# Optimization experiments

Hardware: AMD Instinct MI355X
Metric: run time of the kernel (lower is better)

The kernel has to match this reference:

```python
import jax, jax.numpy as jnp
import numpy as np
from jax.scipy.special import gammaln

NPTS = 100          # hardcoded npts default in the torch module
EPS = 1e-8          # self.epsilon


def _build_grid(K):
    # Static quadrature grids for thresholds t_i = i/K, i=0..K.
    # Original code builds torch.linspace(eps, t_i - eps, int(NPTS * t_i)) per bin;
    # we precompute all K+1 grids padded to NPTS points with a validity mask.
    # (Note: the repo's thresholds arange/K*2-1 in [-1,1] crash torch.linspace for
    # negative b; we use the intended [0,1] Beta support thresholds t_i = i/K.)
    grid = np.full((K + 1, NPTS), 0.5, dtype=np.float32)  # 0.5 pad avoids log(0)
    mask = np.zeros((K + 1, NPTS), dtype=np.float32)
    for i in range(K + 1):
        n = int(NPTS * (i / K))
        if n > 0:
            grid[i, :n] = np.linspace(EPS, i / K - EPS, n, dtype=np.float32)
            mask[i, :n] = 1.0
    return jnp.asarray(grid), jnp.asarray(mask)


def setup_inputs() -> dict:
    key = jax.random.key(0)
    k1, k2, k3 = jax.random.split(key, 3)
    B, C, K = 65536, 512, 10
    x = jax.random.normal(k1, (B, C), dtype=jnp.float32)
    Wa = jax.random.normal(k2, (C, 1), dtype=jnp.float32) / np.sqrt(C)
    ba = jnp.zeros((1,), dtype=jnp.float32)
    Wb = jax.random.normal(k3, (C, 1), dtype=jnp.float32) / np.sqrt(C)
    bb = jnp.zeros((1,), dtype=jnp.float32)
    return {"x": x, "Wa": Wa, "ba": ba, "Wb": Wb, "bb": bb, "num_classes": K}


def reference(x, Wa, ba, Wb, bb, num_classes):
    K = int(num_classes)
    grid, mask = _build_grid(K)                      # [K+1, NPTS]
    # alpha/beta heads: Linear -> Softplus -> 1 + . -> clamp(1, 100)
    alpha = jnp.clip(1.0 + jax.nn.softplus(x @ Wa + ba), 1.0, 100.0)  # [B, 1]
    beta = jnp.clip(1.0 + jax.nn.softplus(x @ Wb + bb), 1.0, 100.0)   # [B, 1]
    a = alpha[:, :, None]                            # [B, 1, 1]
    b = beta[:, :, None]
    # Beta log_prob on all quadrature points: [B, K+1, NPTS]
    log_norm = gammaln(a) + gammaln(b) - gammaln(a + b)
    logpdf = (a - 1.0) * jnp.log(grid) + (b - 1.0) * jnp.log1p(-grid) - log_norm
    dx = 1.0 / (NPTS * K)                            # dx constant from original code
    cdf = jnp.sum(jnp.exp(logpdf) * mask, axis=-1) * dx   # [B, K+1] unnormalized CDFs
    probs = cdf[:, 1:] - cdf[:, :-1]                 # per-bin mass, [B, K]
    # diag(1/rowsum) @ probs  ==  row-normalize
    return probs / jnp.sum(probs, axis=-1, keepdims=True)
```

## Files before the change

### kernel.cpp

```cpp
#include <hip/hip_runtime.h>
#include <math.h>

#define NPTS_C 100
#define EPS_C 1e-8

#if defined(__has_builtin)
# if __has_builtin(__builtin_amdgcn_exp2f)
#  define FAST_EXP2(x) __builtin_amdgcn_exp2f(x)
# else
#  define FAST_EXP2(x) exp2f(x)
# endif
#else
# define FAST_EXP2(x) exp2f(x)
#endif

__device__ __forceinline__ float dot4(float4 a, float4 b) {
    return a.x * b.x + a.y * b.y + a.z * b.z + a.w * b.w;
}

__device__ __forceinline__ float wave_reduce_sum(float v) {
#pragma unroll
    for (int m = 1; m < 64; m <<= 1)
        v += __shfl_xor(v, m, 64);
    return v;
}

constexpr int KC   = 10;
constexpr int NTAB = 550;

__global__ __launch_bounds__(256, 3) void fused512_kernel(
    const float* __restrict__ x, const float* __restrict__ Wa,
    const float* __restrict__ ba, const float* __restrict__ Wb,
    const float* __restrict__ bb, float* __restrict__ out)
{
    __shared__ __align__(16) float2 s_tab[NTAB];
    __shared__ __align__(16) float4 s_w4[256];

    const int tid = threadIdx.x;

    if (tid < 128) {
        s_w4[tid]       = reinterpret_cast<const float4*>(Wa)[tid];
        s_w4[128 + tid] = reinterpret_cast<const float4*>(Wb)[tid];
    }

    {
        int base = 0;
#pragma unroll
        for (int i = 1; i <= KC; ++i) {
            const int n = 10 * i;
            const double start = EPS_C;
            const double stop  = (double)i / (double)KC - EPS_C;
            const double step  = (stop - start) / (double)(n - 1);
            for (int j = tid; j < n; j += 256) {
                const double g = (j == n - 1) ? stop : start + step * (double)j;
                const float g32 = (float)g;
                s_tab[base + j] = make_float2(log2f(g32), log2f(1.0f - g32));
            }
            base += n;
        }
    }
    __syncthreads();

    const int lane = tid & 63;
    const int wv   = tid >> 6;
    const int r8   = lane & 7;
    const int part = lane >> 3;
    const float ba0 = ba[0], bb0 = bb[0];

    const int row = blockIdx.x * 32 + wv * 8 + r8;
    const float* px = x + (size_t)row * 512 + part * 4;

    float4 xv[16];
#pragma unroll
    for (int j = 0; j < 16; ++j)
        xv[j] = *reinterpret_cast<const float4*>(px + (size_t)j * 32);

    float da = 0.f, db = 0.f;
#pragma unroll
    for (int j = 0; j < 16; ++j) {
        const float4 wa = s_w4[part + 8 * j];
        const float4 wb = s_w4[128 + part + 8 * j];
        da += dot4(xv[j], wa);
        db += dot4(xv[j], wb);
    }
    da += __shfl_xor(da, 8, 64);  db += __shfl_xor(db, 8, 64);
    da += __shfl_xor(da, 16, 64); db += __shfl_xor(db, 16, 64);
    da += __shfl_xor(da, 32, 64); db += __shfl_xor(db, 32, 64);
    da += ba0; db += bb0;

    const float sa = fmaxf(da, 0.f) + log1pf(expf(-fabsf(da)));
    const float sb = fmaxf(db, 0.f) + log1pf(expf(-fabsf(db)));
    const float alpha = fminf(fmaxf(1.f + sa, 1.f), 100.f);
    const float beta  = fminf(fmaxf(1.f + sb, 1.f), 100.f);
    const float am1 = alpha - 1.f, bm1 = beta - 1.f;

    const float den = am1 + bm1;
    float m = (den > 0.f) ? am1 / den : 0.5f;
    m = fminf(fmaxf(m, 1e-6f), 1.f - 1e-6f);
    const float M2 = am1 * log2f(m) + bm1 * log2f(1.f - m);

    float seg[KC];
    {
        int base = 0;
#pragma unroll
        for (int i = 1; i <= KC; ++i) {
            const int n = 10 * i;
            float s = 0.f;
            for (int t = part; t < n; t += 8) {
                const float2 e = s_tab[base + t];
                s += FAST_EXP2(fmaf(am1, e.x, fmaf(bm1, e.y, -M2)));
            }
            seg[i - 1] = s;
            base += n;
        }
    }
#pragma unroll
    for (int i = 0; i < KC; ++i) {
        seg[i] += __shfl_xor(seg[i], 8, 64);
        seg[i] += __shfl_xor(seg[i], 16, 64);
        seg[i] += __shfl_xor(seg[i], 32, 64);
    }

    if (part == 0) {
        float* orow = out + (size_t)row * KC;
        const float inv_total = 1.f / seg[KC - 1];
        float prev = 0.f;
        float2* o2 = reinterpret_cast<float2*>(orow);
#pragma unroll
        for (int j = 0; j < KC; j += 2) {
            const float p0 = (seg[j]     - prev)   * inv_total;
            const float p1 = (seg[j + 1] - seg[j]) * inv_total;
            o2[j >> 1] = make_float2(p0, p1);
            prev = seg[j + 1];
        }
    }
}

__global__ __launch_bounds__(256, 4) void ub_fused_kernel(
    const float* __restrict__ x, const float* __restrict__ Wa,
    const float* __restrict__ ba, const float* __restrict__ Wb,
    const float* __restrict__ bb, float* __restrict__ out,
    int B, int C, int K)
{
    __shared__ __align__(16) float s_lg[600];
    __shared__ __align__(16) float s_l1g[600];
    __shared__ __align__(16) float s_w[1024];

    const int tid = threadIdx.x;
    for (int c = tid; c < C; c += blockDim.x) {
        s_w[c]     = Wa[c];
        s_w[C + c] = Wb[c];
    }
    {
        int base = 0;
        for (int i = 1; i <= K; ++i) {
            const int n = (int)((double)NPTS_C * ((double)i / (double)K));
            const double start = EPS_C;
            const double stop  = (double)i / (double)K - EPS_C;
            const double step  = (n > 1) ? (stop - start) / (double)(n - 1) : 0.0;
            for (int j = tid; j < n; j += blockDim.x) {
                float g = (j == n - 1) ? (float)stop : (float)(start + step * (double)j);
                s_lg[base + j]  = logf(g);
                s_l1g[base + j] = log1pf(-g);
            }
            base += n;
        }
    }
    __syncthreads();

    const float ba0 = ba[0], bb0 = bb[0];
    const int wave = tid >> 6;
    const int lane = tid & 63;
    const int wavesPerBlock = blockDim.x >> 6;
    const int waveId = blockIdx.x * wavesPerBlock + wave;
    const int nWaves = gridDim.x * wavesPerBlock;

    for (int row = waveId; row < B; row += nWaves) {
        const float* xr = x + (size_t)row * C;
        float da = 0.f, db = 0.f;
        for (int c0 = 0; c0 < C; c0 += 256) {
            const float4 xv = *reinterpret_cast<const float4*>(xr + c0 + 4 * lane);
            const float4 wa = *reinterpret_cast<const float4*>(&s_w[c0 + 4 * lane]);
            const float4 wb = *reinterpret_cast<const float4*>(&s_w[C + c0 + 4 * lane]);
            da += xv.x * wa.x + xv.y * wa.y + xv.z * wa.z + xv.w * wa.w;
            db += xv.x * wb.x + xv.y * wb.y + xv.z * wb.z + xv.w * wb.w;
        }
        da = wave_reduce_sum(da) + ba0;
        db = wave_reduce_sum(db) + bb0;

        const float sa = fmaxf(da, 0.f) + log1pf(expf(-fabsf(da)));
        const float sb = fmaxf(db, 0.f) + log1pf(expf(-fabsf(db)));
        const float alpha = fminf(fmaxf(1.f + sa, 1.f), 100.f);
        const float beta  = fminf(fmaxf(1.f + sb, 1.f), 100.f);
        const float log_norm = lgammaf(alpha) + lgammaf(beta) - lgammaf(alpha + beta);
        const float am1 = alpha - 1.f, bm1 = beta - 1.f;

        float cdf_prev = 0.f, myp = 0.f;
        int base = 0;
        for (int i = 1; i <= K; ++i) {
            const int n = (int)((double)NPTS_C * ((double)i / (double)K));
            float s = 0.f;
            for (int p = lane; p < n; p += 64) {
                const float lp = fmaf(am1, s_lg[base + p],
                                 fmaf(bm1, s_l1g[base + p], -log_norm));
                s += expf(lp);
            }
            const float cdf = wave_reduce_sum(s);
            if (lane == i - 1) myp = cdf - cdf_prev;
            cdf_prev = cdf;
            base += n;
        }
        if (lane < K)
            out[(size_t)row * K + lane] = myp / cdf_prev;
    }
}

extern "C" void kernel_launch(void* const* d_in, const int* in_sizes, int n_in,
                              void* d_out, int out_size, void* d_ws, size_t ws_size,
                              hipStream_t stream) {
    const float* x  = (const float*)d_in[0];
    const float* Wa = (const float*)d_in[1];
    const float* ba = (const float*)d_in[2];
    const float* Wb = (const float*)d_in[3];
    const float* bb = (const float*)d_in[4];
    float* out = (float*)d_out;

    const int C = in_sizes[1];
    const int B = in_sizes[0] / C;
    const int K = out_size / B;

    const bool fast_ok = (C == 512) && (K == 10) && (B % 32 == 0);

    if (fast_ok) {
        fused512_kernel<<<B / 32, 256, 0, stream>>>(x, Wa, ba, Wb, bb, out);
    } else {
        int nblocks = (B + 3) / 4;
        if (nblocks > 2048) nblocks = 2048;
        ub_fused_kernel<<<nblocks, 256, 0, stream>>>(x, Wa, ba, Wb, bb, out, B, C, K);
    }
}
```

Before: 32.36 us.

## Raise occupancy, stream x loads, use fast exp2/log2 intrinsics, unroll quadrature

Raises the launch-bounds occupancy hint from 3 to 6 blocks per CU. To fit that, the 16 float4 x loads are no longer held all at once in registers; they are consumed two at a time with split accumulators. Softplus and the mode log use the hardware exp2/log2 builtins instead of libm expf/log1pf/log2f, and the inner quadrature loop is unrolled. The intent is more waves in flight to hide memory latency on a bandwidth-bound read of x. The risk is fewer loads outstanding per wave and slightly lower accuracy of softplus for tiny arguments.

Result: slower. 33.91 us (+4.8%).

```diff
diff --git a/kernel.cpp b/kernel.cpp
--- a/kernel.cpp
+++ b/kernel.cpp
@@ -7,12 +7,18 @@
 #if defined(__has_builtin)
 # if __has_builtin(__builtin_amdgcn_exp2f)
 #  define FAST_EXP2(x) __builtin_amdgcn_exp2f(x)
+#  define FAST_LOG2(x) __builtin_amdgcn_logf(x)
 # else
 #  define FAST_EXP2(x) exp2f(x)
+#  define FAST_LOG2(x) log2f(x)
 # endif
 #else
 # define FAST_EXP2(x) exp2f(x)
+# define FAST_LOG2(x) log2f(x)
 #endif
+
+#define LOG2E_F 1.44269504088896340736f
+#define LN2_F   0.69314718055994530942f
 
 __device__ __forceinline__ float dot4(float4 a, float4 b) {
     return a.x * b.x + a.y * b.y + a.z * b.z + a.w * b.w;
@@ -28,7 +34,7 @@
 constexpr int KC   = 10;
 constexpr int NTAB = 550;
 
-__global__ __launch_bounds__(256, 3) void fused512_kernel(
+__global__ __launch_bounds__(256, 6) void fused512_kernel(
     const float* __restrict__ x, const float* __restrict__ Wa,
     const float* __restrict__ ba, const float* __restrict__ Wb,
     const float* __restrict__ bb, float* __restrict__ out)
@@ -70,34 +76,35 @@
     const int row = blockIdx.x * 32 + wv * 8 + r8;
     const float* px = x + (size_t)row * 512 + part * 4;
 
-    float4 xv[16];
-#pragma unroll
-    for (int j = 0; j < 16; ++j)
-        xv[j] = *reinterpret_cast<const float4*>(px + (size_t)j * 32);
-
-    float da = 0.f, db = 0.f;
-#pragma unroll
-    for (int j = 0; j < 16; ++j) {
-        const float4 wa = s_w4[part + 8 * j];
-        const float4 wb = s_w4[128 + part + 8 * j];
-        da += dot4(xv[j], wa);
-        db += dot4(xv[j], wb);
-    }
+    float da = 0.f, db = 0.f, da2 = 0.f, db2 = 0.f;
+#pragma unroll
+    for (int j = 0; j < 16; j += 2) {
+        const float4 x0 = *reinterpret_cast<const float4*>(px + (size_t)j * 32);
+        const float4 x1 = *reinterpret_cast<const float4*>(px + (size_t)(j + 1) * 32);
+        da  += dot4(x0, s_w4[part + 8 * j]);
+        db  += dot4(x0, s_w4[128 + part + 8 * j]);
+        da2 += dot4(x1, s_w4[part + 8 * (j + 1)]);
+        db2 += dot4(x1, s_w4[128 + part + 8 * (j + 1)]);
+    }
+    da += da2; db += db2;
+
     da += __shfl_xor(da, 8, 64);  db += __shfl_xor(db, 8, 64);
     da += __shfl_xor(da, 16, 64); db += __shfl_xor(db, 16, 64);
     da += __shfl_xor(da, 32, 64); db += __shfl_xor(db, 32, 64);
     da += ba0; db += bb0;
 
-    const float sa = fmaxf(da, 0.f) + log1pf(expf(-fabsf(da)));
-    const float sb = fmaxf(db, 0.f) + log1pf(expf(-fabsf(db)));
+    const float ua = FAST_EXP2(-fabsf(da) * LOG2E_F);
+    const float ub = FAST_EXP2(-fabsf(db) * LOG2E_F);
+    const float sa = fmaxf(da, 0.f) + FAST_LOG2(1.f + ua) * LN2_F;
+    const float sb = fmaxf(db, 0.f) + FAST_LOG2(1.f + ub) * LN2_F;
     const float alpha = fminf(fmaxf(1.f + sa, 1.f), 100.f);
     const float beta  = fminf(fmaxf(1.f + sb, 1.f), 100.f);
     const float am1 = alpha - 1.f, bm1 = beta - 1.f;
 
     const float den = am1 + bm1;
-    float m = (den > 0.f) ? am1 / den : 0.5f;
-    m = fminf(fmaxf(m, 1e-6f), 1.f - 1e-6f);
-    const float M2 = am1 * log2f(m) + bm1 * log2f(1.f - m);
+    float mm = (den > 0.f) ? am1 / den : 0.5f;
+    mm = fminf(fmaxf(mm, 1e-6f), 1.f - 1e-6f);
+    const float M2 = am1 * FAST_LOG2(mm) + bm1 * FAST_LOG2(1.f - mm);
 
     float seg[KC];
     {
@@ -106,6 +113,7 @@
         for (int i = 1; i <= KC; ++i) {
             const int n = 10 * i;
             float s = 0.f;
+#pragma unroll
             for (int t = part; t < n; t += 8) {
                 const float2 e = s_tab[base + t];
                 s += FAST_EXP2(fmaf(am1, e.x, fmaf(bm1, e.y, -M2)));
```
